# Optimization experiments

Measured on AMD Instinct MI355X. Metric: run time of the kernel, lower is better.

The kernel has to match this reference:

```python
import jax, jax.numpy as jnp
import numpy as np

N_NODES = 50000
N_EDGES = 1600000
IN_CH = 128
OUT_CH = 128


def setup_inputs() -> dict:
    key = jax.random.key(0)
    k1, k2, k3, k4, k5 = jax.random.split(key, 5)
    x = jax.random.normal(k1, (N_NODES, IN_CH), dtype=jnp.float32)
    # edge_index[0] = destination (row), edge_index[1] = source (col)
    edge_index = jax.random.randint(k2, (2, N_EDGES), 0, N_NODES, dtype=jnp.int64)
    # Linear parameters (PyTorch default init: U(-1/sqrt(fan_in), 1/sqrt(fan_in)))
    bound = 1.0 / np.sqrt(IN_CH)
    W = jax.random.uniform(k3, (OUT_CH, IN_CH), dtype=jnp.float32, minval=-bound, maxval=bound)
    b = jax.random.uniform(k4, (OUT_CH,), dtype=jnp.float32, minval=-bound, maxval=bound)
    return {"x": x, "edge_index": edge_index, "W": W, "b": b}


def reference(x, edge_index, W, b) -> jnp.ndarray:
    # Linear projection: h = x @ W^T + b  -> [N, OUT_CH]
    h = jnp.einsum("nd,od->no", x, W) + b
    # spmm sum aggregation: out[dst] = sum_{edges e: dst(e)=dst} h[src(e)]
    dst = edge_index[0]
    src = edge_index[1]
    out = jax.ops.segment_sum(h[src], dst, num_segments=N_NODES)
    return out
```

## Files before the change

kernel.cpp:

```cpp
#include <hip/hip_runtime.h>

constexpr int N  = 50000;
constexpr int E  = 1600000;
constexpr int CH = 128;

constexpr int BSZ  = 64;
constexpr int NB   = (N + BSZ - 1) / BSZ;
constexpr int CAP  = 2560;
constexpr int PBLK = 512;
constexpr int EPB  = E / PBLK;
constexpr int GEMM_BLOCKS = N / 16;

constexpr size_t H_OFF     = 0;
constexpr size_t H_SZ      = (size_t)N * CH * 2;
constexpr size_t PAIRS_OFF = H_OFF + H_SZ;
constexpr size_t PAIRS_SZ  = (size_t)NB * CAP * 4;
constexpr size_t GCUR_OFF  = PAIRS_OFF + PAIRS_SZ;
constexpr size_t GCUR_SZ   = 3328;
constexpr size_t REQUIRED  = GCUR_OFF + GCUR_SZ;
constexpr size_t FB_REQUIRED = H_SZ;

static __device__ __forceinline__ ushort f2bf(float f) {
    unsigned u = __float_as_uint(f);
    return (ushort)((u + 0x7fffu + ((u >> 16) & 1u)) >> 16);
}
static __device__ __forceinline__ float bf_lo(unsigned u) { return __uint_as_float(u << 16); }
static __device__ __forceinline__ float bf_hi(unsigned u) { return __uint_as_float(u & 0xffff0000u); }

typedef __attribute__((ext_vector_type(8))) short bf16x8;
typedef __attribute__((ext_vector_type(4))) float f32x4;

static __device__ __forceinline__ void gemm_body(int gb, int tid,
                                                 const float* __restrict__ x,
                                                 const float* __restrict__ W,
                                                 const float* __restrict__ bias,
                                                 ushort* __restrict__ h) {
    const int m    = tid & 15;
    const int q    = (tid >> 4) & 3;
    const int wave = tid >> 6;
    const int r0   = gb * 16;
    const int c0   = wave * 32;

    const float* xrow = x + (size_t)(r0 + m) * CH + q * 8;
    const float* wr0  = W + (size_t)(c0 + m) * CH + q * 8;
    const float* wr1  = wr0 + 16 * CH;

    f32x4 acc0 = {0.f, 0.f, 0.f, 0.f};
    f32x4 acc1 = {0.f, 0.f, 0.f, 0.f};

#pragma unroll
    for (int kc = 0; kc < CH; kc += 32) {
        float4 xa = *(const float4*)(xrow + kc);
        float4 xb = *(const float4*)(xrow + kc + 4);
        float4 wa0 = *(const float4*)(wr0 + kc);
        float4 wb0 = *(const float4*)(wr0 + kc + 4);
        float4 wa1 = *(const float4*)(wr1 + kc);
        float4 wb1 = *(const float4*)(wr1 + kc + 4);
        bf16x8 a, b0, b1;
        a[0] = (short)f2bf(xa.x); a[1] = (short)f2bf(xa.y);
        a[2] = (short)f2bf(xa.z); a[3] = (short)f2bf(xa.w);
        a[4] = (short)f2bf(xb.x); a[5] = (short)f2bf(xb.y);
        a[6] = (short)f2bf(xb.z); a[7] = (short)f2bf(xb.w);
        b0[0] = (short)f2bf(wa0.x); b0[1] = (short)f2bf(wa0.y);
        b0[2] = (short)f2bf(wa0.z); b0[3] = (short)f2bf(wa0.w);
        b0[4] = (short)f2bf(wb0.x); b0[5] = (short)f2bf(wb0.y);
        b0[6] = (short)f2bf(wb0.z); b0[7] = (short)f2bf(wb0.w);
        b1[0] = (short)f2bf(wa1.x); b1[1] = (short)f2bf(wa1.y);
        b1[2] = (short)f2bf(wa1.z); b1[3] = (short)f2bf(wa1.w);
        b1[4] = (short)f2bf(wb1.x); b1[5] = (short)f2bf(wb1.y);
        b1[6] = (short)f2bf(wb1.z); b1[7] = (short)f2bf(wb1.w);
        acc0 = __builtin_amdgcn_mfma_f32_16x16x32_bf16(a, b0, acc0, 0, 0, 0);
        acc1 = __builtin_amdgcn_mfma_f32_16x16x32_bf16(a, b1, acc1, 0, 0, 0);
    }

    const int col0 = c0 + m;
    const float bb0 = bias[col0];
    const float bb1 = bias[col0 + 16];
#pragma unroll
    for (int r = 0; r < 4; r++) {
        size_t row = (size_t)(r0 + q * 4 + r) * CH;
        h[row + col0]      = f2bf(acc0[r] + bb0);
        h[row + col0 + 16] = f2bf(acc1[r] + bb1);
    }
}

__global__ __launch_bounds__(256) void gemm_and_scatter(const float* __restrict__ x,
                                                        const float* __restrict__ W,
                                                        const float* __restrict__ bias,
                                                        ushort* __restrict__ h,
                                                        const int* __restrict__ ei,
                                                        int* __restrict__ gcur,
                                                        unsigned* __restrict__ pairs) {
    __shared__ int cnt[NB];
    __shared__ int cur[NB];
    const int bid = blockIdx.x;
    const int tid = threadIdx.x;

    if (bid >= PBLK) {
        gemm_body(bid - PBLK, tid, x, W, bias, h);
        return;
    }

    const int k = bid;
    for (int j = tid; j < NB; j += 256) cnt[j] = 0;
    __syncthreads();
    const int* dp = ei + k * EPB;
    const int* sp = ei + E + k * EPB;
    for (int i = tid; i < EPB; i += 256) atomicAdd(&cnt[dp[i] >> 6], 1);
    __syncthreads();
    for (int j = tid; j < NB; j += 256) {
        int c = cnt[j];
        cur[j] = j * CAP + (c ? atomicAdd(&gcur[j], c) : 0);
    }
    __syncthreads();
    for (int i = tid; i < EPB; i += 256) {
        int d = dp[i], s = sp[i];
        int bb = d >> 6;
        int p = atomicAdd(&cur[bb], 1);
        if (p < (bb + 1) * CAP)
            pairs[p] = ((unsigned)(d & (BSZ - 1)) << 16) | (unsigned)s;
    }
}

__global__ __launch_bounds__(512) void agg_fused(const ushort* __restrict__ h,
                                                 const unsigned* __restrict__ pairs,
                                                 const int* __restrict__ gcur,
                                                 float* __restrict__ out) {
    __shared__ unsigned raw[CAP];
    __shared__ ushort   srt[CAP];
    __shared__ int hist[BSZ], offs[BSZ], cur[BSZ];
    const int b = blockIdx.x, t = threadIdx.x;
    const int cnt = min(gcur[b], CAP);
    const int wave = t >> 6;
    const int lane = t & 63;
    const int quarter = lane >> 4;
    const int cq      = lane & 15;

    const unsigned* slab = pairs + (size_t)b * CAP;
    for (int i = t; i < cnt; i += 512) raw[i] = slab[i];
    if (t < BSZ) hist[t] = 0;
    __syncthreads();
    for (int i = t; i < cnt; i += 512) atomicAdd(&hist[raw[i] >> 16], 1);
    __syncthreads();
    int v = (t < BSZ) ? hist[t] : 0;
    if (t < BSZ) offs[t] = v;
    __syncthreads();
    for (int o = 1; o < BSZ; o <<= 1) {
        int u = 0;
        if (t < BSZ && t >= o) u = offs[t - o];
        __syncthreads();
        if (t < BSZ) offs[t] += u;
        __syncthreads();
    }
    if (t < BSZ) { int excl = offs[t] - v; offs[t] = excl; cur[t] = excl; }
    __syncthreads();
    for (int i = t; i < cnt; i += 512) {
        unsigned w = raw[i];
        int p = atomicAdd(&cur[w >> 16], 1);
        srt[p] = (ushort)(w & 0xffffu);
    }
    __syncthreads();

    const ushort* hp = h + (size_t)cq * 8;

#pragma unroll
    for (int j = 0; j < 8; j++) {
        const int nl = wave * 8 + j;
        const int st = offs[nl];
        const int c  = hist[nl];
        float a0 = 0.f, a1 = 0.f, a2 = 0.f, a3 = 0.f;
        float a4 = 0.f, a5 = 0.f, a6 = 0.f, a7 = 0.f;
        int i = 0;
        for (; i + 16 <= c; i += 16) {
            const int e0 = st + i + quarter;
            int s0 = srt[e0];
            int s1 = srt[e0 + 4];
            int s2 = srt[e0 + 8];
            int s3 = srt[e0 + 12];
            uint4 v0 = *(const uint4*)(hp + (size_t)s0 * CH);
            uint4 v1 = *(const uint4*)(hp + (size_t)s1 * CH);
            uint4 v2 = *(const uint4*)(hp + (size_t)s2 * CH);
            uint4 v3 = *(const uint4*)(hp + (size_t)s3 * CH);
            a0 += bf_lo(v0.x); a1 += bf_hi(v0.x); a2 += bf_lo(v0.y); a3 += bf_hi(v0.y);
            a4 += bf_lo(v0.z); a5 += bf_hi(v0.z); a6 += bf_lo(v0.w); a7 += bf_hi(v0.w);
            a0 += bf_lo(v1.x); a1 += bf_hi(v1.x); a2 += bf_lo(v1.y); a3 += bf_hi(v1.y);
            a4 += bf_lo(v1.z); a5 += bf_hi(v1.z); a6 += bf_lo(v1.w); a7 += bf_hi(v1.w);
            a0 += bf_lo(v2.x); a1 += bf_hi(v2.x); a2 += bf_lo(v2.y); a3 += bf_hi(v2.y);
            a4 += bf_lo(v2.z); a5 += bf_hi(v2.z); a6 += bf_lo(v2.w); a7 += bf_hi(v2.w);
            a0 += bf_lo(v3.x); a1 += bf_hi(v3.x); a2 += bf_lo(v3.y); a3 += bf_hi(v3.y);
            a4 += bf_lo(v3.z); a5 += bf_hi(v3.z); a6 += bf_lo(v3.w); a7 += bf_hi(v3.w);
        }
        for (; i < c; i += 4) {
            if (i + quarter < c) {
                int s = srt[st + i + quarter];
                uint4 vv = *(const uint4*)(hp + (size_t)s * CH);
                a0 += bf_lo(vv.x); a1 += bf_hi(vv.x); a2 += bf_lo(vv.y); a3 += bf_hi(vv.y);
                a4 += bf_lo(vv.z); a5 += bf_hi(vv.z); a6 += bf_lo(vv.w); a7 += bf_hi(vv.w);
            }
        }
        a0 += __shfl_xor(a0, 16); a0 += __shfl_xor(a0, 32);
        a1 += __shfl_xor(a1, 16); a1 += __shfl_xor(a1, 32);
        a2 += __shfl_xor(a2, 16); a2 += __shfl_xor(a2, 32);
        a3 += __shfl_xor(a3, 16); a3 += __shfl_xor(a3, 32);
        a4 += __shfl_xor(a4, 16); a4 += __shfl_xor(a4, 32);
        a5 += __shfl_xor(a5, 16); a5 += __shfl_xor(a5, 32);
        a6 += __shfl_xor(a6, 16); a6 += __shfl_xor(a6, 32);
        a7 += __shfl_xor(a7, 16); a7 += __shfl_xor(a7, 32);
        const int n = b * BSZ + nl;
        if (quarter == 0 && n < N) {
            float* op = out + (size_t)n * CH + cq * 8;
            *(float4*)(op)     = make_float4(a0, a1, a2, a3);
            *(float4*)(op + 4) = make_float4(a4, a5, a6, a7);
        }
    }
}

__global__ __launch_bounds__(256) void gemm_only(const float* __restrict__ x,
                                                 const float* __restrict__ W,
                                                 const float* __restrict__ bias,
                                                 ushort* __restrict__ h) {
    gemm_body(blockIdx.x, threadIdx.x, x, W, bias, h);
}

__global__ void atomic_agg(const ushort* __restrict__ h, const int* __restrict__ ei,
                           float* __restrict__ out) {
    int tid = blockIdx.x * blockDim.x + threadIdx.x;
    int e  = tid >> 5;
    int cg = (tid & 31) * 4;
    if (e < E) {
        int d = ei[e];
        int s = ei[E + e];
        ushort4 v = *(const ushort4*)(h + (size_t)s * CH + cg);
        float* o = out + (size_t)d * CH + cg;
        atomicAdd(o + 0, __uint_as_float((unsigned)v.x << 16));
        atomicAdd(o + 1, __uint_as_float((unsigned)v.y << 16));
        atomicAdd(o + 2, __uint_as_float((unsigned)v.z << 16));
        atomicAdd(o + 3, __uint_as_float((unsigned)v.w << 16));
    }
}

extern "C" void kernel_launch(void* const* d_in, const int* in_sizes, int n_in,
                              void* d_out, int out_size, void* d_ws, size_t ws_size,
                              hipStream_t stream) {
    const float* x  = (const float*)d_in[0];
    const int*   ei = (const int*)d_in[1];
    const float* W  = (const float*)d_in[2];
    const float* b  = (const float*)d_in[3];
    float* out = (float*)d_out;

    char* ws = (char*)d_ws;
    ushort* h = (ushort*)(ws + H_OFF);

    if (ws_size >= REQUIRED) {
        unsigned* pairs = (unsigned*)(ws + PAIRS_OFF);
        int*      gcur  = (int*)(ws + GCUR_OFF);

        hipMemsetAsync(gcur, 0, NB * sizeof(int), stream);
        gemm_and_scatter<<<PBLK + GEMM_BLOCKS, 256, 0, stream>>>(x, W, b, h, ei, gcur, pairs);
        agg_fused<<<NB, 512, 0, stream>>>(h, pairs, gcur, out);
    } else if (ws_size >= FB_REQUIRED) {
        gemm_only<<<GEMM_BLOCKS, 256, 0, stream>>>(x, W, b, h);
        hipMemsetAsync(out, 0, (size_t)out_size * sizeof(float), stream);
        int total = E * 32;
        atomic_agg<<<(total + 255) / 256, 256, 0, stream>>>(h, ei, out);
    }
}
```

Before: 199.0 us.

## Locally sort scatter edges in LDS before writing coalesced bucket runs

The partition blocks now stage their edge chunk in shared memory, build a per-bucket prefix scan, and counting-sort edges locally so that global writes to each bucket's slab come out as contiguous runs instead of random scattered stores. The number of partition blocks is halved so each handles twice as many edges, which reduces global atomics on the bucket counters. The packed word now also carries the bucket id, and the aggregation kernel masks it off. This costs a much larger LDS footprint per block (about 38KB) and extra sync and scan steps, and leaves fewer partition blocks running concurrently with the GEMM blocks.

```diff
diff --git a/kernel.cpp b/kernel.cpp
--- a/kernel.cpp
+++ b/kernel.cpp
@@ -7,7 +7,7 @@
 constexpr int BSZ  = 64;
 constexpr int NB   = (N + BSZ - 1) / BSZ;
 constexpr int CAP  = 2560;
-constexpr int PBLK = 512;
+constexpr int PBLK = 256;
 constexpr int EPB  = E / PBLK;
 constexpr int GEMM_BLOCKS = N / 16;
 
@@ -91,8 +91,13 @@
                                                         const int* __restrict__ ei,
                                                         int* __restrict__ gcur,
                                                         unsigned* __restrict__ pairs) {
+    __shared__ unsigned raw[EPB];
+    __shared__ ushort   srt16[EPB];
     __shared__ int cnt[NB];
+    __shared__ int lstart[NB];
+    __shared__ int gpos[NB];
     __shared__ int cur[NB];
+    __shared__ int ssum[256];
     const int bid = blockIdx.x;
     const int tid = threadIdx.x;
 
@@ -102,23 +107,58 @@
     }
 
     const int k = bid;
-    for (int j = tid; j < NB; j += 256) cnt[j] = 0;
-    __syncthreads();
     const int* dp = ei + k * EPB;
     const int* sp = ei + E + k * EPB;
-    for (int i = tid; i < EPB; i += 256) atomicAdd(&cnt[dp[i] >> 6], 1);
-    __syncthreads();
+
+    for (int j = tid; j < NB; j += 256) cnt[j] = 0;
+    for (int i = tid; i < EPB; i += 256) {
+        int d = dp[i], s = sp[i];
+        raw[i] = ((unsigned)(d >> 6) << 22) | ((unsigned)(d & (BSZ - 1)) << 16) | (unsigned)s;
+    }
+    __syncthreads();
+
+    for (int i = tid; i < EPB; i += 256) atomicAdd(&cnt[raw[i] >> 22], 1);
+    __syncthreads();
+
     for (int j = tid; j < NB; j += 256) {
         int c = cnt[j];
-        cur[j] = j * CAP + (c ? atomicAdd(&gcur[j], c) : 0);
-    }
-    __syncthreads();
+        gpos[j] = j * CAP + (c ? atomicAdd(&gcur[j], c) : 0);
+    }
+
+    {
+        const int base = tid * 4;
+        int s = 0;
+#pragma unroll
+        for (int i = 0; i < 4; i++) { int j = base + i; if (j < NB) s += cnt[j]; }
+        ssum[tid] = s;
+        __syncthreads();
+        for (int o = 1; o < 256; o <<= 1) {
+            int u = (tid >= o) ? ssum[tid - o] : 0;
+            __syncthreads();
+            ssum[tid] += u;
+            __syncthreads();
+        }
+        int run = ssum[tid] - s;
+#pragma unroll
+        for (int i = 0; i < 4; i++) {
+            int j = base + i;
+            if (j < NB) { lstart[j] = run; cur[j] = run; run += cnt[j]; }
+        }
+    }
+    __syncthreads();
+
     for (int i = tid; i < EPB; i += 256) {
-        int d = dp[i], s = sp[i];
-        int bb = d >> 6;
-        int p = atomicAdd(&cur[bb], 1);
-        if (p < (bb + 1) * CAP)
-            pairs[p] = ((unsigned)(d & (BSZ - 1)) << 16) | (unsigned)s;
+        int p = atomicAdd(&cur[raw[i] >> 22], 1);
+        srt16[p] = (ushort)i;
+    }
+    __syncthreads();
+
+    for (int i = tid; i < EPB; i += 256) {
+        unsigned w = raw[srt16[i]];
+        int bkt = w >> 22;
+        int gdst = gpos[bkt] + (i - lstart[bkt]);
+        if (gdst < (bkt + 1) * CAP)
+            pairs[gdst] = w;
     }
 }
 
@@ -140,7 +180,7 @@
     for (int i = t; i < cnt; i += 512) raw[i] = slab[i];
     if (t < BSZ) hist[t] = 0;
     __syncthreads();
-    for (int i = t; i < cnt; i += 512) atomicAdd(&hist[raw[i] >> 16], 1);
+    for (int i = t; i < cnt; i += 512) atomicAdd(&hist[(raw[i] >> 16) & (BSZ - 1)], 1);
     __syncthreads();
     int v = (t < BSZ) ? hist[t] : 0;
     if (t < BSZ) offs[t] = v;
@@ -156,7 +196,7 @@
     __syncthreads();
     for (int i = t; i < cnt; i += 512) {
         unsigned w = raw[i];
-        int p = atomicAdd(&cur[w >> 16], 1);
+        int p = atomicAdd(&cur[(w >> 16) & (BSZ - 1)], 1);
         srt[p] = (ushort)(w & 0xffffu);
     }
     __syncthreads();
```

New measurement: 178.7 us. 1.11x faster.
